# Kernel optimization log

Hardware: AMD Instinct MI355X
Metric: run time of the kernel (lower is better)

## Reference

```python
import jax, jax.numpy as jnp
import numpy as np

B, N, IN_FEAT, OUT_FEAT, FEAT_DIM, N_HEAD = 16, 1024, 64, 128, 64, 4
NEG_SLOPE = 0.2


def setup_inputs() -> dict:
    key = jax.random.key(0)
    k1, k2, k3, k4 = jax.random.split(key, 4)
    # xavier-uniform-ish init, gain folded into scale
    def xav(k, shape):
        fan_in, fan_out = shape[-2], shape[-1]
        lim = 1.414 * np.sqrt(6.0 / (fan_in + fan_out))
        return jax.random.uniform(k, shape, jnp.float32, -lim, lim)
    return {
        "h": jax.random.normal(k1, (B, N, IN_FEAT), jnp.float32),
        "mask": jnp.ones((B, 1, N, N), jnp.float32),
        "w": xav(k2, (N_HEAD, IN_FEAT, OUT_FEAT)),
        "a_src": xav(k3, (N_HEAD, OUT_FEAT, FEAT_DIM)),
        "a_dst": xav(k4, (N_HEAD, OUT_FEAT, FEAT_DIM)),
        "bias": jnp.zeros((OUT_FEAT,), jnp.float32),
    }


def reference(h, mask, w, a_src, a_dst, bias):
    # h: [B,N,F_in]; w: [H,F_in,F_out] -> h_prime: [B,H,N,F_out]
    h_prime = jnp.einsum('bnf,hfo->bhno', h, w)
    attn_src = jnp.einsum('bhno,hod->bhnd', h_prime, a_src)  # [B,H,N,D]
    attn_dst = jnp.einsum('bhno,hod->bhnd', h_prime, a_dst)  # [B,H,N,D]
    scores = jnp.einsum('bhnd,bhmd->bhnm', attn_src, attn_dst)  # [B,H,N,N]
    attn = jax.nn.softmax(jax.nn.leaky_relu(scores, NEG_SLOPE), axis=-1)
    # dropout is identity in eval mode (deterministic reference)
    attn = attn * mask  # mask broadcast over heads
    out = jnp.einsum('bhnm,bhmo->bno', attn, h_prime) + bias  # sum over heads
    out = out + h_prime.sum(axis=1)  # skip connection
    return out, attn
```

## Files before the change

kernel.cpp:

```cpp
#include <hip/hip_runtime.h>

#define BB 16
#define NN 1024
#define FIN 64
#define FOUT 128
#define DD 64
#define HH 4
#define NEG 0.2f

#define RT 32
#define CT 128

typedef __attribute__((ext_vector_type(8))) short short8;
typedef __attribute__((ext_vector_type(4))) float f32x4;

__device__ __forceinline__ unsigned short f2bf(float x) {
    union { float f; unsigned u; } v; v.f = x;
    unsigned r = v.u + 0x7fffu + ((v.u >> 16) & 1u);
    return (unsigned short)(r >> 16);
}
__device__ __forceinline__ float bf2f(unsigned short s) {
    union { float f; unsigned u; } v; v.u = ((unsigned)s) << 16;
    return v.f;
}

#define MFMA(a, b, c) __builtin_amdgcn_mfma_f32_16x16x32_bf16((a), (b), (c), 0, 0, 0)

__global__ __launch_bounds__(256) void gat_k1(
    const float* __restrict__ h,
    const float* __restrict__ w,
    const float* __restrict__ a_src,
    const float* __restrict__ a_dst,
    unsigned short* __restrict__ asHg,
    unsigned short* __restrict__ asLg,
    unsigned short* __restrict__ adHg,
    unsigned short* __restrict__ adLg,
    unsigned short* __restrict__ hpTg,
    float* __restrict__ hpsum)
{
    __shared__ float hL[RT][FIN + 1];
    __shared__ float wL[FIN][FOUT + 2];
    __shared__ float hpL[RT][FOUT + 2];

    const int t  = threadIdx.x;
    const int tx = t & 31;
    const int ty = t >> 5;
    const int blk = blockIdx.x;
    const int b   = blk / (NN / RT);
    const int n0  = (blk % (NN / RT)) * RT;

    for (int idx = t; idx < RT * FIN / 4; idx += 256) {
        int r = (idx * 4) / FIN;
        int f = (idx * 4) % FIN;
        float4 v = *reinterpret_cast<const float4*>(&h[((size_t)b * NN + n0 + r) * FIN + f]);
        hL[r][f + 0] = v.x; hL[r][f + 1] = v.y; hL[r][f + 2] = v.z; hL[r][f + 3] = v.w;
    }

    float sum_acc[4][4];
#pragma unroll
    for (int i = 0; i < 4; i++)
#pragma unroll
        for (int j = 0; j < 4; j++) sum_acc[i][j] = 0.f;

    for (int hh = 0; hh < HH; ++hh) {
        __syncthreads();
        for (int idx = t; idx < FIN * FOUT / 4; idx += 256) {
            int k = (idx * 4) / FOUT;
            int o = (idx * 4) % FOUT;
            float4 v = *reinterpret_cast<const float4*>(&w[((size_t)hh * FIN + k) * FOUT + o]);
            wL[k][o + 0] = v.x; wL[k][o + 1] = v.y; wL[k][o + 2] = v.z; wL[k][o + 3] = v.w;
        }
        __syncthreads();

        float acc[4][4];
#pragma unroll
        for (int i = 0; i < 4; i++)
#pragma unroll
            for (int j = 0; j < 4; j++) acc[i][j] = 0.f;

#pragma unroll 8
        for (int k = 0; k < FIN; k++) {
            float av0 = hL[ty][k], av1 = hL[ty + 8][k], av2 = hL[ty + 16][k], av3 = hL[ty + 24][k];
            float bv0 = wL[k][tx], bv1 = wL[k][tx + 32], bv2 = wL[k][tx + 64], bv3 = wL[k][tx + 96];
            acc[0][0] += av0 * bv0; acc[0][1] += av0 * bv1; acc[0][2] += av0 * bv2; acc[0][3] += av0 * bv3;
            acc[1][0] += av1 * bv0; acc[1][1] += av1 * bv1; acc[1][2] += av1 * bv2; acc[1][3] += av1 * bv3;
            acc[2][0] += av2 * bv0; acc[2][1] += av2 * bv1; acc[2][2] += av2 * bv2; acc[2][3] += av2 * bv3;
            acc[3][0] += av3 * bv0; acc[3][1] += av3 * bv1; acc[3][2] += av3 * bv2; acc[3][3] += av3 * bv3;
        }

        const size_t bh = (size_t)b * HH + hh;
#pragma unroll
        for (int i = 0; i < 4; i++) {
            int r = i * 8 + ty;
#pragma unroll
            for (int j = 0; j < 4; j++) {
                int o = j * 32 + tx;
                hpL[r][o] = acc[i][j];
                sum_acc[i][j] += acc[i][j];
            }
        }
        __syncthreads();

        float as0[4], as1[4], ad0[4], ad1[4];
#pragma unroll
        for (int i = 0; i < 4; i++) { as0[i] = 0.f; as1[i] = 0.f; ad0[i] = 0.f; ad1[i] = 0.f; }

#pragma unroll 4
        for (int o = 0; o < FOUT; o++) {
            size_t aoff = ((size_t)hh * FOUT + o) * DD;
            float sv0 = a_src[aoff + tx];
            float sv1 = a_src[aoff + tx + 32];
            float dv0 = a_dst[aoff + tx];
            float dv1 = a_dst[aoff + tx + 32];
#pragma unroll
            for (int i = 0; i < 4; i++) {
                float hv = hpL[i * 8 + ty][o];
                as0[i] += hv * sv0; as1[i] += hv * sv1;
                ad0[i] += hv * dv0; ad1[i] += hv * dv1;
            }
        }
#pragma unroll
        for (int i = 0; i < 4; i++) {
            int r = i * 8 + ty;
            size_t base = (bh * NN + n0 + r) * DD;
            unsigned short h0, h1;
            h0 = f2bf(as0[i]); asHg[base + tx]      = h0; asLg[base + tx]      = f2bf(as0[i] - bf2f(h0));
            h1 = f2bf(as1[i]); asHg[base + tx + 32] = h1; asLg[base + tx + 32] = f2bf(as1[i] - bf2f(h1));
            h0 = f2bf(ad0[i]); adHg[base + tx]      = h0; adLg[base + tx]      = f2bf(ad0[i] - bf2f(h0));
            h1 = f2bf(ad1[i]); adHg[base + tx + 32] = h1; adLg[base + tx + 32] = f2bf(ad1[i] - bf2f(h1));
        }

        {
            int o = t & 127, half = t >> 7;
            size_t dst = (bh * FOUT + o) * NN + n0 + half * 16;
            short8 v0, v1;
#pragma unroll
            for (int k = 0; k < 8; k++) v0[k] = (short)f2bf(hpL[half * 16 + k][o]);
#pragma unroll
            for (int k = 0; k < 8; k++) v1[k] = (short)f2bf(hpL[half * 16 + 8 + k][o]);
            *reinterpret_cast<short8*>(&hpTg[dst])     = v0;
            *reinterpret_cast<short8*>(&hpTg[dst + 8]) = v1;
        }
    }

#pragma unroll
    for (int i = 0; i < 4; i++) {
        int r = i * 8 + ty;
        size_t rowoff = ((size_t)b * NN + n0 + r) * FOUT;
#pragma unroll
        for (int j = 0; j < 4; j++) {
            hpsum[rowoff + j * 32 + tx] = sum_acc[i][j];
        }
    }
}

__global__ __launch_bounds__(256) void gat_k2(
    const float* __restrict__ mask,
    const float* __restrict__ bias,
    const unsigned short* __restrict__ asHg,
    const unsigned short* __restrict__ asLg,
    const unsigned short* __restrict__ adHg,
    const unsigned short* __restrict__ adLg,
    const unsigned short* __restrict__ hpTg,
    const float* __restrict__ hpsum,
    float* __restrict__ out,
    float* __restrict__ attn)
{
    __shared__ __align__(16) unsigned short adHs[CT * 64];
    __shared__ __align__(16) unsigned short adLs[CT * 64];
    __shared__ __align__(16) unsigned short asHs[RT * 64];
    __shared__ __align__(16) unsigned short asLs[RT * 64];
    __shared__ __align__(16) unsigned short pBs[RT * 128];
    __shared__ __align__(16) unsigned short hpTs[128 * 64];
    __shared__ float2 red[4][32];

    const int t  = threadIdx.x;
    const int l  = t & 63;
    const int w  = t >> 6;
    const int li = l & 15;
    const int g  = l >> 4;
    const int b  = blockIdx.x / (NN / RT);
    const int n0 = (blockIdx.x % (NN / RT)) * RT;

    f32x4 oacc[2][2];
#pragma unroll
    for (int rf = 0; rf < 2; rf++)
#pragma unroll
        for (int of = 0; of < 2; of++) oacc[rf][of] = f32x4{0.f, 0.f, 0.f, 0.f};

    for (int hh = 0; hh < HH; hh++) {
        const size_t bh = (size_t)b * HH + hh;
        __syncthreads();
        {
            int r = t >> 3, j = t & 7;
            size_t src = (bh * NN + n0 + r) * DD + j * 8;
            int dst = r * 64 + ((j ^ (r & 7)) * 8);
            *reinterpret_cast<short8*>(&asHs[dst]) = *reinterpret_cast<const short8*>(&asHg[src]);
            *reinterpret_cast<short8*>(&asLs[dst]) = *reinterpret_cast<const short8*>(&asLg[src]);
        }
        __syncthreads();

        short8 aH[2][2], aL[2][2];
#pragma unroll
        for (int rf = 0; rf < 2; rf++)
#pragma unroll
            for (int ks = 0; ks < 2; ks++) {
                int r = rf * 16 + li;
                int off = r * 64 + ((ks * 32 + g * 8) ^ ((r & 7) * 8));
                aH[rf][ks] = *reinterpret_cast<const short8*>(&asHs[off]);
                aL[rf][ks] = *reinterpret_cast<const short8*>(&asLs[off]);
            }

        float mreg[2][4], lreg[2][4];
#pragma unroll
        for (int rf = 0; rf < 2; rf++)
#pragma unroll
            for (int q = 0; q < 4; q++) { mreg[rf][q] = -3.0e38f; lreg[rf][q] = 0.f; }

        for (int ct = 0; ct < NN / CT; ct++) {
            __syncthreads();
#pragma unroll
            for (int i = 0; i < 4; i++) {
                int q = t + i * 256;
                int r = q >> 3, j = q & 7;
                size_t src = (bh * NN + (size_t)ct * CT + r) * DD + j * 8;
                int dst = r * 64 + ((j ^ (r & 7)) * 8);
                *reinterpret_cast<short8*>(&adHs[dst]) = *reinterpret_cast<const short8*>(&adHg[src]);
                *reinterpret_cast<short8*>(&adLs[dst]) = *reinterpret_cast<const short8*>(&adLg[src]);
            }
            __syncthreads();

            short8 bH[2][2], bL[2][2];
#pragma unroll
            for (int cf = 0; cf < 2; cf++)
#pragma unroll
                for (int ks = 0; ks < 2; ks++) {
                    int c = w * 32 + cf * 16 + li;
                    int off = c * 64 + ((ks * 32 + g * 8) ^ ((c & 7) * 8));
                    bH[cf][ks] = *reinterpret_cast<const short8*>(&adHs[off]);
                    bL[cf][ks] = *reinterpret_cast<const short8*>(&adLs[off]);
                }
            f32x4 sacc[2][2];
#pragma unroll
            for (int rf = 0; rf < 2; rf++)
#pragma unroll
                for (int cf = 0; cf < 2; cf++) sacc[rf][cf] = f32x4{0.f, 0.f, 0.f, 0.f};
#pragma unroll
            for (int ks = 0; ks < 2; ks++)
#pragma unroll
                for (int rf = 0; rf < 2; rf++)
#pragma unroll
                    for (int cf = 0; cf < 2; cf++) {
                        sacc[rf][cf] = MFMA(aH[rf][ks], bH[cf][ks], sacc[rf][cf]);
                        sacc[rf][cf] = MFMA(aH[rf][ks], bL[cf][ks], sacc[rf][cf]);
                        sacc[rf][cf] = MFMA(aL[rf][ks], bH[cf][ks], sacc[rf][cf]);
                    }
#pragma unroll
            for (int rf = 0; rf < 2; rf++)
#pragma unroll
                for (int q = 0; q < 4; q++) {
                    float v0 = sacc[rf][0][q]; v0 = v0 > 0.f ? v0 : NEG * v0;
                    float v1 = sacc[rf][1][q]; v1 = v1 > 0.f ? v1 : NEG * v1;
                    float nm = fmaxf(mreg[rf][q], fmaxf(v0, v1));
                    lreg[rf][q] = lreg[rf][q] * __expf(mreg[rf][q] - nm)
                                + __expf(v0 - nm) + __expf(v1 - nm);
                    mreg[rf][q] = nm;
                }
        }

#pragma unroll
        for (int rf = 0; rf < 2; rf++)
#pragma unroll
            for (int q = 0; q < 4; q++) {
                float m = mreg[rf][q], lv = lreg[rf][q];
#pragma unroll
                for (int msk = 1; msk < 16; msk <<= 1) {
                    float om = __shfl_xor(m, msk);
                    float ol = __shfl_xor(lv, msk);
                    float nm = fmaxf(m, om);
                    lv = lv * __expf(m - nm) + ol * __expf(om - nm);
                    m = nm;
                }
                mreg[rf][q] = m; lreg[rf][q] = lv;
            }
        if (li == 0) {
#pragma unroll
            for (int rf = 0; rf < 2; rf++)
#pragma unroll
                for (int q = 0; q < 4; q++)
                    red[w][rf * 16 + g * 4 + q] = make_float2(mreg[rf][q], lreg[rf][q]);
        }
        __syncthreads();
        float mf[2][4], linv[2][4];
#pragma unroll
        for (int rf = 0; rf < 2; rf++)
#pragma unroll
            for (int q = 0; q < 4; q++) {
                int row = rf * 16 + g * 4 + q;
                float2 r0 = red[0][row], r1 = red[1][row], r2 = red[2][row], r3 = red[3][row];
                float m = fmaxf(fmaxf(r0.x, r1.x), fmaxf(r2.x, r3.x));
                float lv = r0.y * __expf(r0.x - m) + r1.y * __expf(r1.x - m)
                         + r2.y * __expf(r2.x - m) + r3.y * __expf(r3.x - m);
                mf[rf][q] = m;
                linv[rf][q] = 1.0f / lv;
            }

        for (int ct = 0; ct < NN / CT; ct++) {
            __syncthreads();
#pragma unroll
            for (int i = 0; i < 4; i++) {
                int q = t + i * 256;
                int r = q >> 3, j = q & 7;
                size_t src = (bh * NN + (size_t)ct * CT + r) * DD + j * 8;
                int dst = r * 64 + ((j ^ (r & 7)) * 8);
                *reinterpret_cast<short8*>(&adHs[dst]) = *reinterpret_cast<const short8*>(&adHg[src]);
                *reinterpret_cast<short8*>(&adLs[dst]) = *reinterpret_cast<const short8*>(&adLg[src]);
            }
            __syncthreads();

            short8 bH[2][2], bL[2][2];
#pragma unroll
            for (int cf = 0; cf < 2; cf++)
#pragma unroll
                for (int ks = 0; ks < 2; ks++) {
                    int c = w * 32 + cf * 16 + li;
                    int off = c * 64 + ((ks * 32 + g * 8) ^ ((c & 7) * 8));
                    bH[cf][ks] = *reinterpret_cast<const short8*>(&adHs[off]);
                    bL[cf][ks] = *reinterpret_cast<const short8*>(&adLs[off]);
                }
            f32x4 sacc[2][2];
#pragma unroll
            for (int rf = 0; rf < 2; rf++)
#pragma unroll
                for (int cf = 0; cf < 2; cf++) sacc[rf][cf] = f32x4{0.f, 0.f, 0.f, 0.f};
#pragma unroll
            for (int ks = 0; ks < 2; ks++)
#pragma unroll
                for (int rf = 0; rf < 2; rf++)
#pragma unroll
                    for (int cf = 0; cf < 2; cf++) {
                        sacc[rf][cf] = MFMA(aH[rf][ks], bH[cf][ks], sacc[rf][cf]);
                        sacc[rf][cf] = MFMA(aH[rf][ks], bL[cf][ks], sacc[rf][cf]);
                        sacc[rf][cf] = MFMA(aL[rf][ks], bH[cf][ks], sacc[rf][cf]);
                    }
#pragma unroll
            for (int rf = 0; rf < 2; rf++)
#pragma unroll
                for (int cf = 0; cf < 2; cf++)
#pragma unroll
                    for (int q = 0; q < 4; q++) {
                        float v = sacc[rf][cf][q];
                        v = v > 0.f ? v : NEG * v;
                        float p = __expf(v - mf[rf][q]) * linv[rf][q];
                        int row = rf * 16 + g * 4 + q;
                        int c = w * 32 + cf * 16 + li;
                        pBs[row * 128 + (c ^ ((row & 15) * 8))] = f2bf(p);
                    }
            __syncthreads();
            {
                int row = t >> 3, cb = (t & 7) * 16;
                int o0 = row * 128 + ((cb)     ^ ((row & 15) * 8));
                int o1 = row * 128 + ((cb + 8) ^ ((row & 15) * 8));
                short8 p0 = *reinterpret_cast<short8*>(&pBs[o0]);
                short8 p1 = *reinterpret_cast<short8*>(&pBs[o1]);
                const float* mp = mask + ((size_t)b * NN + n0 + row) * NN + (size_t)ct * CT + cb;
                float* ap = attn + (bh * NN + n0 + row) * NN + (size_t)ct * CT + cb;
                float pv[16];
#pragma unroll
                for (int k = 0; k < 8; k++) pv[k]     = bf2f((unsigned short)p0[k]);
#pragma unroll
                for (int k = 0; k < 8; k++) pv[k + 8] = bf2f((unsigned short)p1[k]);
#pragma unroll
                for (int k4 = 0; k4 < 4; k4++) {
                    float4 mv = *reinterpret_cast<const float4*>(&mp[k4 * 4]);
                    float4 av;
                    av.x = pv[k4 * 4 + 0] * mv.x; av.y = pv[k4 * 4 + 1] * mv.y;
                    av.z = pv[k4 * 4 + 2] * mv.z; av.w = pv[k4 * 4 + 3] * mv.w;
                    *reinterpret_cast<float4*>(&ap[k4 * 4]) = av;
                    pv[k4 * 4 + 0] = av.x; pv[k4 * 4 + 1] = av.y;
                    pv[k4 * 4 + 2] = av.z; pv[k4 * 4 + 3] = av.w;
                }
                short8 q0, q1;
#pragma unroll
                for (int k = 0; k < 8; k++) { q0[k] = (short)f2bf(pv[k]); q1[k] = (short)f2bf(pv[k + 8]); }
                *reinterpret_cast<short8*>(&pBs[o0]) = q0;
                *reinterpret_cast<short8*>(&pBs[o1]) = q1;
            }
#pragma unroll
            for (int s = 0; s < 2; s++) {
                __syncthreads();
#pragma unroll
                for (int i = 0; i < 4; i++) {
                    int q = t + i * 256;
                    int o = q >> 3, j = q & 7;
                    size_t src = (bh * FOUT + o) * NN + (size_t)ct * CT + s * 64 + j * 8;
                    int dst = o * 64 + ((j ^ (o & 7)) * 8);
                    *reinterpret_cast<short8*>(&hpTs[dst]) = *reinterpret_cast<const short8*>(&hpTg[src]);
                }
                __syncthreads();
                short8 pa[2][2], hb[2][2];
#pragma unroll
                for (int rf = 0; rf < 2; rf++)
#pragma unroll
                    for (int kc = 0; kc < 2; kc++) {
                        int r = rf * 16 + li;
                        int k = s * 64 + kc * 32 + g * 8;
                        pa[rf][kc] = *reinterpret_cast<const short8*>(&pBs[r * 128 + (k ^ ((r & 15) * 8))]);
                    }
#pragma unroll
                for (int of = 0; of < 2; of++)
#pragma unroll
                    for (int kc = 0; kc < 2; kc++) {
                        int o = w * 32 + of * 16 + li;
                        int k = kc * 32 + g * 8;
                        hb[of][kc] = *reinterpret_cast<const short8*>(&hpTs[o * 64 + (k ^ ((o & 7) * 8))]);
                    }
#pragma unroll
                for (int kc = 0; kc < 2; kc++)
#pragma unroll
                    for (int rf = 0; rf < 2; rf++)
#pragma unroll
                        for (int of = 0; of < 2; of++)
                            oacc[rf][of] = MFMA(pa[rf][kc], hb[of][kc], oacc[rf][of]);
            }
        }
    }

    __syncthreads();
    float* outL = reinterpret_cast<float*>(hpTs);
#pragma unroll
    for (int rf = 0; rf < 2; rf++)
#pragma unroll
        for (int of = 0; of < 2; of++)
#pragma unroll
            for (int q = 0; q < 4; q++) {
                int row = rf * 16 + g * 4 + q;
                int col = w * 32 + of * 16 + li;
                outL[row * 128 + col] = oacc[rf][of][q];
            }
    __syncthreads();
    {
        int row = t >> 3, cb = (t & 7) * 16;
        size_t obase = ((size_t)b * NN + n0 + row) * FOUT + cb;
#pragma unroll
        for (int k4 = 0; k4 < 4; k4++) {
            float4 v  = *reinterpret_cast<float4*>(&outL[row * 128 + cb + k4 * 4]);
            float4 bs = *reinterpret_cast<const float4*>(&bias[cb + k4 * 4]);
            float4 hs = *reinterpret_cast<const float4*>(&hpsum[obase + k4 * 4]);
            v.x += bs.x + hs.x; v.y += bs.y + hs.y; v.z += bs.z + hs.z; v.w += bs.w + hs.w;
            *reinterpret_cast<float4*>(&out[obase + k4 * 4]) = v;
        }
    }
}

extern "C" void kernel_launch(void* const* d_in, const int* in_sizes, int n_in,
                              void* d_out, int out_size, void* d_ws, size_t ws_size,
                              hipStream_t stream) {
    const float* h      = (const float*)d_in[0];
    const float* mask   = (const float*)d_in[1];
    const float* w      = (const float*)d_in[2];
    const float* a_src  = (const float*)d_in[3];
    const float* a_dst  = (const float*)d_in[4];
    const float* bias   = (const float*)d_in[5];

    float* out  = (float*)d_out;
    float* attn = out + (size_t)BB * NN * FOUT;

    const size_t NASD = (size_t)BB * HH * NN * DD;
    unsigned short* asHg = (unsigned short*)d_ws;
    unsigned short* asLg = asHg + NASD;
    unsigned short* adHg = asLg + NASD;
    unsigned short* adLg = adHg + NASD;
    unsigned short* hpTg = adLg + NASD;
    float* hpsum = (float*)(hpTg + (size_t)BB * HH * FOUT * NN);

    dim3 grid(BB * (NN / RT));
    dim3 block(256);
    gat_k1<<<grid, block, 0, stream>>>(h, w, a_src, a_dst, asHg, asLg, adHg, adLg, hpTg, hpsum);
    gat_k2<<<grid, block, 0, stream>>>(mask, bias, asHg, asLg, adHg, adLg, hpTg, hpsum, out, attn);
}
```

Baseline: 316.8 us.

## Use direct global-to-LDS loads, drop hp/as LDS staging, remap blocks

Stages the attn_dst tiles with global_load_lds, which writes into LDS without going through registers. The attn_src fragments and the h_prime^T B-operand are now loaded straight from global memory, so their LDS buffers and several barriers go away. The red and outL scratch buffers now alias existing LDS arrays. Other changes: an occupancy hint of 4 blocks in launch_bounds, s_setprio around the MFMA groups, and a block-index swizzle that spreads batches across XCDs. The risks are uncoalesced per-lane global reads for hpT and extra L2 traffic in exchange for less LDS use and higher occupancy.

```diff
diff --git a/kernel.cpp b/kernel.cpp
--- a/kernel.cpp
+++ b/kernel.cpp
@@ -154,7 +154,57 @@
     }
 }
 
-__global__ __launch_bounds__(256) void gat_k2(
+__device__ __forceinline__ void stage_tile(
+    const unsigned short* gH, const unsigned short* gL,
+    unsigned short* sH, unsigned short* sL, int w, int l)
+{
+#pragma unroll
+    for (int i = 0; i < 4; i++) {
+        int c = i * 256 + w * 64 + l;
+        int r = c >> 3;
+        int j = (c & 7) ^ (r & 7);
+        const unsigned short* srcH = gH + r * DD + j * 8;
+        const unsigned short* srcL = gL + r * DD + j * 8;
+        unsigned short* dH = sH + (size_t)(i * 256 + w * 64) * 8;
+        unsigned short* dL = sL + (size_t)(i * 256 + w * 64) * 8;
+        __builtin_amdgcn_global_load_lds(
+            (const __attribute__((address_space(1))) unsigned int*)srcH,
+            (__attribute__((address_space(3))) unsigned int*)dH, 16, 0, 0);
+        __builtin_amdgcn_global_load_lds(
+            (const __attribute__((address_space(1))) unsigned int*)srcL,
+            (__attribute__((address_space(3))) unsigned int*)dL, 16, 0, 0);
+    }
+}
+
+__device__ __forceinline__ void score_tile(
+    const unsigned short* adHs, const unsigned short* adLs,
+    const short8 aH[2][2], const short8 aL[2][2],
+    int w, int li, int g, f32x4 sacc[2][2])
+{
+#pragma unroll
+    for (int ks = 0; ks < 2; ks++) {
+        short8 bH[2], bL[2];
+#pragma unroll
+        for (int cf = 0; cf < 2; cf++) {
+            int c = w * 32 + cf * 16 + li;
+            int off = c * 64 + ((ks * 32 + g * 8) ^ ((c & 7) * 8));
+            bH[cf] = *reinterpret_cast<const short8*>(&adHs[off]);
+            bL[cf] = *reinterpret_cast<const short8*>(&adLs[off]);
+        }
+        __builtin_amdgcn_s_setprio(1);
+#pragma unroll
+        for (int rf = 0; rf < 2; rf++)
+#pragma unroll
+            for (int cf = 0; cf < 2; cf++) {
+                sacc[rf][cf] = MFMA(aH[rf][ks], bH[cf], sacc[rf][cf]);
+                sacc[rf][cf] = MFMA(aH[rf][ks], bL[cf], sacc[rf][cf]);
+                sacc[rf][cf] = MFMA(aL[rf][ks], bH[cf], sacc[rf][cf]);
+            }
+        __builtin_amdgcn_s_setprio(0);
+    }
+}
+
+__global__ __launch_bounds__(256, 4) void gat_k2(
     const float* __restrict__ mask,
     const float* __restrict__ bias,
     const unsigned short* __restrict__ asHg,
@@ -168,19 +218,20 @@
 {
     __shared__ __align__(16) unsigned short adHs[CT * 64];
     __shared__ __align__(16) unsigned short adLs[CT * 64];
-    __shared__ __align__(16) unsigned short asHs[RT * 64];
-    __shared__ __align__(16) unsigned short asLs[RT * 64];
     __shared__ __align__(16) unsigned short pBs[RT * 128];
-    __shared__ __align__(16) unsigned short hpTs[128 * 64];
-    __shared__ float2 red[4][32];
+
+    float2* red  = reinterpret_cast<float2*>(pBs);
+    float*  outL = reinterpret_cast<float*>(adHs);
 
     const int t  = threadIdx.x;
     const int l  = t & 63;
     const int w  = t >> 6;
     const int li = l & 15;
     const int g  = l >> 4;
-    const int b  = blockIdx.x / (NN / RT);
-    const int n0 = (blockIdx.x % (NN / RT)) * RT;
+
+    const int lb = (blockIdx.x & 7) * 64 + (blockIdx.x >> 3);
+    const int b  = lb >> 5;
+    const int n0 = (lb & 31) * RT;
 
     f32x4 oacc[2][2];
 #pragma unroll
@@ -190,25 +241,15 @@
 
     for (int hh = 0; hh < HH; hh++) {
         const size_t bh = (size_t)b * HH + hh;
-        __syncthreads();
-        {
-            int r = t >> 3, j = t & 7;
-            size_t src = (bh * NN + n0 + r) * DD + j * 8;
-            int dst = r * 64 + ((j ^ (r & 7)) * 8);
-            *reinterpret_cast<short8*>(&asHs[dst]) = *reinterpret_cast<const short8*>(&asHg[src]);
-            *reinterpret_cast<short8*>(&asLs[dst]) = *reinterpret_cast<const short8*>(&asLg[src]);
-        }
-        __syncthreads();
 
         short8 aH[2][2], aL[2][2];
 #pragma unroll
         for (int rf = 0; rf < 2; rf++)
 #pragma unroll
             for (int ks = 0; ks < 2; ks++) {
-                int r = rf * 16 + li;
-                int off = r * 64 + ((ks * 32 + g * 8) ^ ((r & 7) * 8));
-                aH[rf][ks] = *reinterpret_cast<const short8*>(&asHs[off]);
-                aL[rf][ks] = *reinterpret_cast<const short8*>(&asLs[off]);
+                size_t src = (bh * NN + n0 + rf * 16 + li) * DD + ks * 32 + g * 8;
+                aH[rf][ks] = *reinterpret_cast<const short8*>(&asHg[src]);
+                aL[rf][ks] = *reinterpret_cast<const short8*>(&asLg[src]);
             }
 
         float mreg[2][4], lreg[2][4];
@@ -219,42 +260,17 @@
 
         for (int ct = 0; ct < NN / CT; ct++) {
             __syncthreads();
-#pragma unroll
-            for (int i = 0; i < 4; i++) {
-                int q = t + i * 256;
-                int r = q >> 3, j = q & 7;
-                size_t src = (bh * NN + (size_t)ct * CT + r) * DD + j * 8;
-                int dst = r * 64 + ((j ^ (r & 7)) * 8);
-                *reinterpret_cast<short8*>(&adHs[dst]) = *reinterpret_cast<const short8*>(&adHg[src]);
-                *reinterpret_cast<short8*>(&adLs[dst]) = *reinterpret_cast<const short8*>(&adLg[src]);
-            }
-            __syncthreads();
-
-            short8 bH[2][2], bL[2][2];
-#pragma unroll
-            for (int cf = 0; cf < 2; cf++)
-#pragma unroll
-                for (int ks = 0; ks < 2; ks++) {
-                    int c = w * 32 + cf * 16 + li;
-                    int off = c * 64 + ((ks * 32 + g * 8) ^ ((c & 7) * 8));
-                    bH[cf][ks] = *reinterpret_cast<const short8*>(&adHs[off]);
-                    bL[cf][ks] = *reinterpret_cast<const short8*>(&adLs[off]);
-                }
+            stage_tile(adHg + (bh * NN + (size_t)ct * CT) * DD,
+                       adLg + (bh * NN + (size_t)ct * CT) * DD, adHs, adLs, w, l);
+            __syncthreads();
+
             f32x4 sacc[2][2];
 #pragma unroll
             for (int rf = 0; rf < 2; rf++)
 #pragma unroll
                 for (int cf = 0; cf < 2; cf++) sacc[rf][cf] = f32x4{0.f, 0.f, 0.f, 0.f};
-#pragma unroll
-            for (int ks = 0; ks < 2; ks++)
-#pragma unroll
-                for (int rf = 0; rf < 2; rf++)
-#pragma unroll
-                    for (int cf = 0; cf < 2; cf++) {
-                        sacc[rf][cf] = MFMA(aH[rf][ks], bH[cf][ks], sacc[rf][cf]);
-                        sacc[rf][cf] = MFMA(aH[rf][ks], bL[cf][ks], sacc[rf][cf]);
-                        sacc[rf][cf] = MFMA(aL[rf][ks], bH[cf][ks], sacc[rf][cf]);
-                    }
+            score_tile(adHs, adLs, aH, aL, w, li, g, sacc);
+
 #pragma unroll
             for (int rf = 0; rf < 2; rf++)
 #pragma unroll
@@ -283,12 +299,13 @@
                 }
                 mreg[rf][q] = m; lreg[rf][q] = lv;
             }
+        __syncthreads();
         if (li == 0) {
 #pragma unroll
             for (int rf = 0; rf < 2; rf++)
 #pragma unroll
                 for (int q = 0; q < 4; q++)
-                    red[w][rf * 16 + g * 4 + q] = make_float2(mreg[rf][q], lreg[rf][q]);
+                    red[w * 32 + rf * 16 + g * 4 + q] = make_float2(mreg[rf][q], lreg[rf][q]);
         }
         __syncthreads();
         float mf[2][4], linv[2][4];
@@ -297,7 +314,7 @@
 #pragma unroll
             for (int q = 0; q < 4; q++) {
                 int row = rf * 16 + g * 4 + q;
-                float2 r0 = red[0][row], r1 = red[1][row], r2 = red[2][row], r3 = red[3][row];
+                float2 r0 = red[row], r1 = red[32 + row], r2 = red[64 + row], r3 = red[96 + row];
                 float m = fmaxf(fmaxf(r0.x, r1.x), fmaxf(r2.x, r3.x));
                 float lv = r0.y * __expf(r0.x - m) + r1.y * __expf(r1.x - m)
                          + r2.y * __expf(r2.x - m) + r3.y * __expf(r3.x - m);
@@ -307,42 +324,17 @@
 
         for (int ct = 0; ct < NN / CT; ct++) {
             __syncthreads();
-#pragma unroll
-            for (int i = 0; i < 4; i++) {
-                int q = t + i * 256;
-                int r = q >> 3, j = q & 7;
-                size_t src = (bh * NN + (size_t)ct * CT + r) * DD + j * 8;
-                int dst = r * 64 + ((j ^ (r & 7)) * 8);
-                *reinterpret_cast<short8*>(&adHs[dst]) = *reinterpret_cast<const short8*>(&adHg[src]);
-                *reinterpret_cast<short8*>(&adLs[dst]) = *reinterpret_cast<const short8*>(&adLg[src]);
-            }
-            __syncthreads();
-
-            short8 bH[2][2], bL[2][2];
-#pragma unroll
-            for (int cf = 0; cf < 2; cf++)
-#pragma unroll
-                for (int ks = 0; ks < 2; ks++) {
-                    int c = w * 32 + cf * 16 + li;
-                    int off = c * 64 + ((ks * 32 + g * 8) ^ ((c & 7) * 8));
-                    bH[cf][ks] = *reinterpret_cast<const short8*>(&adHs[off]);
-                    bL[cf][ks] = *reinterpret_cast<const short8*>(&adLs[off]);
-                }
+            stage_tile(adHg + (bh * NN + (size_t)ct * CT) * DD,
+                       adLg + (bh * NN + (size_t)ct * CT) * DD, adHs, adLs, w, l);
+            __syncthreads();
+
             f32x4 sacc[2][2];
 #pragma unroll
             for (int rf = 0; rf < 2; rf++)
 #pragma unroll
                 for (int cf = 0; cf < 2; cf++) sacc[rf][cf] = f32x4{0.f, 0.f, 0.f, 0.f};
-#pragma unroll
-            for (int ks = 0; ks < 2; ks++)
-#pragma unroll
-                for (int rf = 0; rf < 2; rf++)
-#pragma unroll
-                    for (int cf = 0; cf < 2; cf++) {
-                        sacc[rf][cf] = MFMA(aH[rf][ks], bH[cf][ks], sacc[rf][cf]);
-                        sacc[rf][cf] = MFMA(aH[rf][ks], bL[cf][ks], sacc[rf][cf]);
-                        sacc[rf][cf] = MFMA(aL[rf][ks], bH[cf][ks], sacc[rf][cf]);
-                    }
+            score_tile(adHs, adLs, aH, aL, w, li, g, sacc);
+
 #pragma unroll
             for (int rf = 0; rf < 2; rf++)
 #pragma unroll
@@ -357,6 +349,7 @@
                         pBs[row * 128 + (c ^ ((row & 15) * 8))] = f2bf(p);
                     }
             __syncthreads();
+
             {
                 int row = t >> 3, cb = (t & 7) * 16;
                 int o0 = row * 128 + ((cb)     ^ ((row & 15) * 8));
@@ -386,48 +379,35 @@
                 *reinterpret_cast<short8*>(&pBs[o0]) = q0;
                 *reinterpret_cast<short8*>(&pBs[o1]) = q1;
             }
-#pragma unroll
-            for (int s = 0; s < 2; s++) {
-                __syncthreads();
-#pragma unroll
-                for (int i = 0; i < 4; i++) {
-                    int q = t + i * 256;
-                    int o = q >> 3, j = q & 7;
-                    size_t src = (bh * FOUT + o) * NN + (size_t)ct * CT + s * 64 + j * 8;
-                    int dst = o * 64 + ((j ^ (o & 7)) * 8);
-                    *reinterpret_cast<short8*>(&hpTs[dst]) = *reinterpret_cast<const short8*>(&hpTg[src]);
+            __syncthreads();
+
+            const unsigned short* hpb = hpTg + (bh * FOUT) * NN + (size_t)ct * CT;
+#pragma unroll
+            for (int kc = 0; kc < 4; kc++) {
+                short8 pa[2], hb[2];
+#pragma unroll
+                for (int rf = 0; rf < 2; rf++) {
+                    int r = rf * 16 + li;
+                    int k = kc * 32 + g * 8;
+                    pa[rf] = *reinterpret_cast<const short8*>(&pBs[r * 128 + (k ^ ((r & 15) * 8))]);
                 }
-                __syncthreads();
-                short8 pa[2][2], hb[2][2];
+#pragma unroll
+                for (int of = 0; of < 2; of++) {
+                    int o = w * 32 + of * 16 + li;
+                    hb[of] = *reinterpret_cast<const short8*>(&hpb[(size_t)o * NN + kc * 32 + g * 8]);
+                }
+                __builtin_amdgcn_s_setprio(1);
 #pragma unroll
                 for (int rf = 0; rf < 2; rf++)
 #pragma unroll
-                    for (int kc = 0; kc < 2; kc++) {
-                        int r = rf * 16 + li;
-                        int k = s * 64 + kc * 32 + g * 8;
-                        pa[rf][kc] = *reinterpret_cast<const short8*>(&pBs[r * 128 + (k ^ ((r & 15) * 8))]);
-                    }
-#pragma unroll
-                for (int of = 0; of < 2; of++)
-#pragma unroll
-                    for (int kc = 0; kc < 2; kc++) {
-                        int o = w * 32 + of * 16 + li;
-                        int k = kc * 32 + g * 8;
-                        hb[of][kc] = *reinterpret_cast<const short8*>(&hpTs[o * 64 + (k ^ ((o & 7) * 8))]);
-                    }
-#pragma unroll
-                for (int kc = 0; kc < 2; kc++)
-#pragma unroll
-                    for (int rf = 0; rf < 2; rf++)
-#pragma unroll
-                        for (int of = 0; of < 2; of++)
-                            oacc[rf][of] = MFMA(pa[rf][kc], hb[of][kc], oacc[rf][of]);
+                    for (int of = 0; of < 2; of++)
+                        oacc[rf][of] = MFMA(pa[rf], hb[of], oacc[rf][of]);
+                __builtin_amdgcn_s_setprio(0);
             }
         }
     }
 
     __syncthreads();
-    float* outL = reinterpret_cast<float*>(hpTs);
 #pragma unroll
     for (int rf = 0; rf < 2; rf++)
 #pragma unroll
```

New measurement: 524.2 us. 1.65x slower.
